# Kernel tuning notes

Measured on AMD Instinct MI355X. Metric: run time of the kernel, lower is better.

The kernel has to match this reference:

```python
import jax, jax.numpy as jnp
import numpy as np

NUM_EMBEDDINGS = 1024
EMBEDDING_DIM = 64
BETA = 0.25


def setup_inputs() -> dict:
    key = jax.random.key(0)
    k1, k2 = jax.random.split(key)
    z = jax.random.normal(k1, (64, 32, 32, EMBEDDING_DIM), dtype=jnp.float32)
    emb = jax.random.uniform(
        k2, (NUM_EMBEDDINGS, EMBEDDING_DIM), dtype=jnp.float32,
        minval=-1.0 / NUM_EMBEDDINGS, maxval=1.0 / NUM_EMBEDDINGS)
    return {"z": z, "emb": emb}


def reference(z, emb):
    zf = z.reshape(-1, EMBEDDING_DIM)                      # [N, D]
    # squared L2 distances via ||z||^2 - 2 z.e + ||e||^2  -> [N, K]
    distances = (jnp.sum(zf * zf, axis=1, keepdims=True)
                 - 2.0 * jnp.matmul(zf, emb.T)
                 + jnp.sum(emb * emb, axis=1))
    encoding_indices = jnp.argmin(distances, axis=1)       # [N]
    quantized = emb[encoding_indices].reshape(z.shape)     # [B, H, W, D]
    commitment_loss = BETA * jnp.mean((jax.lax.stop_gradient(quantized) - z) ** 2)
    codebook_loss = jnp.mean((quantized - jax.lax.stop_gradient(z)) ** 2)
    loss = commitment_loss + codebook_loss
    # straight-through estimator
    quantized = z + jax.lax.stop_gradient(quantized - z)
    return (quantized, loss)
```

## Files before the change

kernel.cpp:

```cpp
#include <hip/hip_runtime.h>
#include <stdint.h>

#define N_ROWS 65536
#define K_CODES 1024
#define D 64
#define OUT_ELEMS 4194304
#define LOSS_SCALE (1.25f / 4194304.0f)
#define ROWS_PER_BLOCK 128
#define GRID_DIST (N_ROWS / ROWS_PER_BLOCK)

typedef short short8 __attribute__((ext_vector_type(8)));
typedef float f32x4 __attribute__((ext_vector_type(4)));

__device__ __forceinline__ unsigned short f2bf(float f) {
    unsigned int u = __float_as_uint(f);
    return (unsigned short)((u + 0x7fffu + ((u >> 16) & 1u)) >> 16);
}

#define ECH (K_CODES * D / 8)
__global__ __launch_bounds__(256) void prep_kernel(const float* __restrict__ emb,
                                                   unsigned short* __restrict__ ebm2,
                                                   float* __restrict__ e2) {
    int t = blockIdx.x * 256 + threadIdx.x;
    if (t < ECH) {
        const float4* s = (const float4*)emb;
        float4 a = s[2 * t], b = s[2 * t + 1];
        uint4 o;
        o.x = f2bf(-2.f * a.x) | ((unsigned int)f2bf(-2.f * a.y) << 16);
        o.y = f2bf(-2.f * a.z) | ((unsigned int)f2bf(-2.f * a.w) << 16);
        o.z = f2bf(-2.f * b.x) | ((unsigned int)f2bf(-2.f * b.y) << 16);
        o.w = f2bf(-2.f * b.z) | ((unsigned int)f2bf(-2.f * b.w) << 16);
        ((uint4*)ebm2)[t] = o;
    } else if (t < ECH + K_CODES) {
        int k = t - ECH;
        const float4* e4 = (const float4*)emb;
        float s = 0.f;
#pragma unroll
        for (int i = 0; i < 16; i++) {
            float4 v = e4[k * 16 + i];
            s += v.x * v.x + v.y * v.y + v.z * v.z + v.w * v.w;
        }
        e2[k] = s;
    }
}

__global__ __launch_bounds__(256) void dist_fused_kernel(
        const float* __restrict__ z, const unsigned short* __restrict__ ebm2,
        const float* __restrict__ e2, const float* __restrict__ emb,
        float* __restrict__ out, float* __restrict__ partials) {
    const int tid = threadIdx.x;
    const int wave = tid >> 6, lane = tid & 63;
    const int n = lane & 15, q = lane >> 4;
    const int block_row0 = blockIdx.x * ROWS_PER_BLOCK;

    short8 b[2][2];
#pragma unroll
    for (int rs = 0; rs < 2; rs++) {
        const float* zr = z + (size_t)(block_row0 + wave * 32 + rs * 16 + n) * D + q * 8;
        float4 f0 = *(const float4*)(zr);
        float4 f1 = *(const float4*)(zr + 4);
        float4 f2 = *(const float4*)(zr + 32);
        float4 f3 = *(const float4*)(zr + 36);
        short8 lo, hi;
        lo[0] = f2bf(f0.x); lo[1] = f2bf(f0.y); lo[2] = f2bf(f0.z); lo[3] = f2bf(f0.w);
        lo[4] = f2bf(f1.x); lo[5] = f2bf(f1.y); lo[6] = f2bf(f1.z); lo[7] = f2bf(f1.w);
        hi[0] = f2bf(f2.x); hi[1] = f2bf(f2.y); hi[2] = f2bf(f2.z); hi[3] = f2bf(f2.w);
        hi[4] = f2bf(f3.x); hi[5] = f2bf(f3.y); hi[6] = f2bf(f3.z); hi[7] = f2bf(f3.w);
        b[rs][0] = lo; b[rs][1] = hi;
    }

    float bestd[2] = {INFINITY, INFINITY};
    int bestk[2] = {0, 0};

    short8 A0a, A1a, A0b, A1b;
    f32x4 Ea, Eb;
    {
        const unsigned short* er0 = ebm2 + (size_t)n * D + q * 8;
        A0a = *(const short8*)er0; A1a = *(const short8*)(er0 + 32);
        Ea = *(const f32x4*)(e2 + q * 4);
        const unsigned short* er1 = ebm2 + (size_t)(16 + n) * D + q * 8;
        A0b = *(const short8*)er1; A1b = *(const short8*)(er1 + 32);
        Eb = *(const f32x4*)(e2 + 16 + q * 4);
    }

    auto step = [&](int t, short8& A0, short8& A1, f32x4& E) {
        f32x4 acc0 = E, acc1 = E;
        acc0 = __builtin_amdgcn_mfma_f32_16x16x32_bf16(A0, b[0][0], acc0, 0, 0, 0);
        acc0 = __builtin_amdgcn_mfma_f32_16x16x32_bf16(A1, b[0][1], acc0, 0, 0, 0);
        acc1 = __builtin_amdgcn_mfma_f32_16x16x32_bf16(A0, b[1][0], acc1, 0, 0, 0);
        acc1 = __builtin_amdgcn_mfma_f32_16x16x32_bf16(A1, b[1][1], acc1, 0, 0, 0);
        int tp = (t + 2 > 63) ? 63 : (t + 2);
        const unsigned short* er = ebm2 + (size_t)(tp * 16 + n) * D + q * 8;
        A0 = *(const short8*)er;
        A1 = *(const short8*)(er + 32);
        E = *(const f32x4*)(e2 + tp * 16 + q * 4);
#pragma unroll
        for (int r = 0; r < 4; r++) {
            float d0 = acc0[r];
            if (d0 < bestd[0]) { bestd[0] = d0; bestk[0] = t * 16 + q * 4 + r; }
            float d1 = acc1[r];
            if (d1 < bestd[1]) { bestd[1] = d1; bestk[1] = t * 16 + q * 4 + r; }
        }
    };

    for (int t = 0; t < 64; t += 2) {
        step(t, A0a, A1a, Ea);
        step(t + 1, A0b, A1b, Eb);
    }

    __shared__ int sh_idx[ROWS_PER_BLOCK];
#pragma unroll
    for (int rs = 0; rs < 2; rs++) {
        unsigned int db = __float_as_uint(bestd[rs]);
        db = (db & 0x80000000u) ? ~db : (db | 0x80000000u);
        unsigned long long key = ((unsigned long long)db << 32) | (unsigned int)bestk[rs];
        unsigned long long o = __shfl_xor(key, 16, 64); key = o < key ? o : key;
        o = __shfl_xor(key, 32, 64); key = o < key ? o : key;
        if (q == 0) sh_idx[wave * 32 + rs * 16 + n] = (int)(key & 0xFFFFFFFFu);
    }
    __syncthreads();

    float ssum = 0.f;
    const float4* z4 = (const float4*)z;
    float4* o4 = (float4*)out;
#pragma unroll
    for (int it = 0; it < 8; it++) {
        int c = it * 256 + tid;
        int lrow = c >> 4, d4 = c & 15;
        int k = sh_idx[lrow];
        size_t gi = (size_t)block_row0 * 16 + c;
        float4 qv = ((const float4*)emb)[k * 16 + d4];
        float4 zv = z4[gi];
        o4[gi] = qv;
        float dx = qv.x - zv.x, dy = qv.y - zv.y, dz = qv.z - zv.z, dw = qv.w - zv.w;
        ssum += dx * dx + dy * dy + dz * dz + dw * dw;
    }
#pragma unroll
    for (int off = 32; off > 0; off >>= 1)
        ssum += __shfl_down(ssum, off, 64);
    __shared__ float ps[4];
    if (lane == 0) ps[wave] = ssum;
    __syncthreads();
    if (tid == 0) partials[blockIdx.x] = ps[0] + ps[1] + ps[2] + ps[3];
}

__global__ __launch_bounds__(256) void loss_kernel(const float* __restrict__ partials,
                                                   float* __restrict__ loss) {
    float s = partials[threadIdx.x] + partials[threadIdx.x + 256];
#pragma unroll
    for (int off = 32; off > 0; off >>= 1)
        s += __shfl_down(s, off, 64);
    __shared__ float ps[4];
    int wave = threadIdx.x >> 6, lane = threadIdx.x & 63;
    if (lane == 0) ps[wave] = s;
    __syncthreads();
    if (threadIdx.x == 0) loss[0] = (ps[0] + ps[1] + ps[2] + ps[3]) * LOSS_SCALE;
}

extern "C" void kernel_launch(void* const* d_in, const int* in_sizes, int n_in,
                              void* d_out, int out_size, void* d_ws, size_t ws_size,
                              hipStream_t stream) {
    const float* z = (const float*)d_in[0];
    const float* emb = (const float*)d_in[1];
    float* out = (float*)d_out;
    float* loss = out + OUT_ELEMS;

    char* ws = (char*)d_ws;
    float* e2 = (float*)ws;
    unsigned short* ebm2 = (unsigned short*)(ws + 4096);
    float* partials = (float*)(ws + 4096 + 131072 + 8192);

    prep_kernel<<<(ECH + K_CODES + 255) / 256, 256, 0, stream>>>(emb, ebm2, e2);
    dist_fused_kernel<<<GRID_DIST, 256, 0, stream>>>(z, ebm2, e2, emb, out, partials);
    loss_kernel<<<1, 256, 0, stream>>>(partials, loss);
}
```

Measured before the change: 109.8 us.

## Stage codebook into LDS via async global_load_lds with XOR swizzle double buffering

The kernel no longer has each wave read bf16 codebook fragments straight from global memory. It now copies the whole codebook into 64KB of shared memory in four 32KB chunks with global_load_lds, double-buffered, and uses an XOR swizzle to avoid bank conflicts on the MFMA operand reads. The goal is to cut redundant L2/global traffic, since all four waves previously fetched the same codebook rows. In exchange it adds block-wide barriers per chunk and a large LDS footprint, which caps occupancy at about two blocks per CU. It also reuses the staging buffer for the index and partial-sum scratch.

Measured after the change: 90.53 us. 1.21x faster.

```diff
diff --git a/kernel.cpp b/kernel.cpp
--- a/kernel.cpp
+++ b/kernel.cpp
@@ -16,6 +16,10 @@
     unsigned int u = __float_as_uint(f);
     return (unsigned short)((u + 0x7fffu + ((u >> 16) & 1u)) >> 16);
 }
+
+#define GLOAD_LDS16(g, l)                                                          \
+    __builtin_amdgcn_global_load_lds((const __attribute__((address_space(1))) void*)(g), \
+                                     (__attribute__((address_space(3))) void*)(l), 16, 0, 0)
 
 #define ECH (K_CODES * D / 8)
 __global__ __launch_bounds__(256) void prep_kernel(const float* __restrict__ emb,
@@ -44,13 +48,14 @@
     }
 }
 
-__global__ __launch_bounds__(256) void dist_fused_kernel(
+__global__ __launch_bounds__(256, 2) void dist_fused_kernel(
         const float* __restrict__ z, const unsigned short* __restrict__ ebm2,
         const float* __restrict__ e2, const float* __restrict__ emb,
         float* __restrict__ out, float* __restrict__ partials) {
+    __shared__ __align__(16) char smem[65536];
     const int tid = threadIdx.x;
     const int wave = tid >> 6, lane = tid & 63;
-    const int n = lane & 15, q = lane >> 4;
+    const int n = lane & 15, q = lane >> 4, nb = n & 7;
     const int block_row0 = blockIdx.x * ROWS_PER_BLOCK;
 
     short8 b[2][2];
@@ -69,46 +74,58 @@
         b[rs][0] = lo; b[rs][1] = hi;
     }
 
+    auto stage = [&](int c) {
+        const int bufoff = (c & 1) << 15;
+        const uint4* gsrc = (const uint4*)ebm2;
+#pragma unroll
+        for (int r = 0; r < 8; r++) {
+            int S = c * 2048 + r * 256 + tid;
+            int P = (S & ~7) | ((S & 7) ^ ((S >> 3) & 7));
+            char* l = smem + bufoff + (r * 256 + (tid & ~63)) * 16;
+            GLOAD_LDS16(gsrc + P, l);
+        }
+    };
+
+    f32x4 Ea = *(const f32x4*)(e2 + q * 4);
+    f32x4 Eb = *(const f32x4*)(e2 + 16 + q * 4);
+    const int base0 = n * 128 + ((q ^ nb) << 4);
+    const int base1 = n * 128 + (((4 | q) ^ nb) << 4);
+
     float bestd[2] = {INFINITY, INFINITY};
     int bestk[2] = {0, 0};
 
-    short8 A0a, A1a, A0b, A1b;
-    f32x4 Ea, Eb;
-    {
-        const unsigned short* er0 = ebm2 + (size_t)n * D + q * 8;
-        A0a = *(const short8*)er0; A1a = *(const short8*)(er0 + 32);
-        Ea = *(const f32x4*)(e2 + q * 4);
-        const unsigned short* er1 = ebm2 + (size_t)(16 + n) * D + q * 8;
-        A0b = *(const short8*)er1; A1b = *(const short8*)(er1 + 32);
-        Eb = *(const f32x4*)(e2 + 16 + q * 4);
+    stage(0);
+    __syncthreads();
+    for (int c = 0; c < 4; c++) {
+        if (c < 3) stage(c + 1);
+        const char* buf = smem + ((c & 1) << 15);
+#pragma unroll
+        for (int tl = 0; tl < 16; tl++) {
+            const int t = c * 16 + tl;
+            short8 a0 = *(const short8*)(buf + tl * 2048 + base0);
+            short8 a1 = *(const short8*)(buf + tl * 2048 + base1);
+            f32x4 E = (tl & 1) ? Eb : Ea;
+            f32x4 acc0 = E, acc1 = E;
+            acc0 = __builtin_amdgcn_mfma_f32_16x16x32_bf16(a0, b[0][0], acc0, 0, 0, 0);
+            acc0 = __builtin_amdgcn_mfma_f32_16x16x32_bf16(a1, b[0][1], acc0, 0, 0, 0);
+            acc1 = __builtin_amdgcn_mfma_f32_16x16x32_bf16(a0, b[1][0], acc1, 0, 0, 0);
+            acc1 = __builtin_amdgcn_mfma_f32_16x16x32_bf16(a1, b[1][1], acc1, 0, 0, 0);
+            int tp = (t + 2 > 63) ? 63 : (t + 2);
+            f32x4 En = *(const f32x4*)(e2 + tp * 16 + q * 4);
+            if (tl & 1) Eb = En; else Ea = En;
+#pragma unroll
+            for (int r = 0; r < 4; r++) {
+                float d0 = acc0[r];
+                if (d0 < bestd[0]) { bestd[0] = d0; bestk[0] = t * 16 + q * 4 + r; }
+                float d1 = acc1[r];
+                if (d1 < bestd[1]) { bestd[1] = d1; bestk[1] = t * 16 + q * 4 + r; }
+            }
+        }
+        __syncthreads();
     }
 
-    auto step = [&](int t, short8& A0, short8& A1, f32x4& E) {
-        f32x4 acc0 = E, acc1 = E;
-        acc0 = __builtin_amdgcn_mfma_f32_16x16x32_bf16(A0, b[0][0], acc0, 0, 0, 0);
-        acc0 = __builtin_amdgcn_mfma_f32_16x16x32_bf16(A1, b[0][1], acc0, 0, 0, 0);
-        acc1 = __builtin_amdgcn_mfma_f32_16x16x32_bf16(A0, b[1][0], acc1, 0, 0, 0);
-        acc1 = __builtin_amdgcn_mfma_f32_16x16x32_bf16(A1, b[1][1], acc1, 0, 0, 0);
-        int tp = (t + 2 > 63) ? 63 : (t + 2);
-        const unsigned short* er = ebm2 + (size_t)(tp * 16 + n) * D + q * 8;
-        A0 = *(const short8*)er;
-        A1 = *(const short8*)(er + 32);
-        E = *(const f32x4*)(e2 + tp * 16 + q * 4);
-#pragma unroll
-        for (int r = 0; r < 4; r++) {
-            float d0 = acc0[r];
-            if (d0 < bestd[0]) { bestd[0] = d0; bestk[0] = t * 16 + q * 4 + r; }
-            float d1 = acc1[r];
-            if (d1 < bestd[1]) { bestd[1] = d1; bestk[1] = t * 16 + q * 4 + r; }
-        }
-    };
-
-    for (int t = 0; t < 64; t += 2) {
-        step(t, A0a, A1a, Ea);
-        step(t + 1, A0b, A1b, Eb);
-    }
-
-    __shared__ int sh_idx[ROWS_PER_BLOCK];
+    int* sh_idx = (int*)smem;
+    float* ps = (float*)(smem + 512);
 #pragma unroll
     for (int rs = 0; rs < 2; rs++) {
         unsigned int db = __float_as_uint(bestd[rs]);
@@ -125,10 +142,10 @@
     float4* o4 = (float4*)out;
 #pragma unroll
     for (int it = 0; it < 8; it++) {
-        int c = it * 256 + tid;
-        int lrow = c >> 4, d4 = c & 15;
+        int cidx = it * 256 + tid;
+        int lrow = cidx >> 4, d4 = cidx & 15;
         int k = sh_idx[lrow];
-        size_t gi = (size_t)block_row0 * 16 + c;
+        size_t gi = (size_t)block_row0 * 16 + cidx;
         float4 qv = ((const float4*)emb)[k * 16 + d4];
         float4 zv = z4[gi];
         o4[gi] = qv;
@@ -138,7 +155,6 @@
 #pragma unroll
     for (int off = 32; off > 0; off >>= 1)
         ssum += __shfl_down(ssum, off, 64);
-    __shared__ float ps[4];
     if (lane == 0) ps[wave] = ssum;
     __syncthreads();
     if (tid == 0) partials[blockIdx.x] = ps[0] + ps[1] + ps[2] + ps[3];
```

## Hold codebook slice in registers per wave and stream z rows through it

Applied to the files above, without the earlier changes.

Removes the prep kernel. Each wave now converts its own quarter of the codebook to bf16 (scaled by -2) and computes the code norms, keeping the result in registers. The block then loops over 16-row chunks of z, and the four waves' partial argmins are combined through shared memory using packed distance|index keys. Quantized rows come from emb, and the loss is taken from the minimum distance instead of recomputing (q-z)^2. This saves a launch and the z re-read, but the distance keys lose mantissa precision (low 10 bits replaced by the index, plus a +1 offset), so argmin ties and the loss are approximated.

After: 113.9 us. 3.7% more time.

```diff
diff --git a/kernel.cpp b/kernel.cpp
--- a/kernel.cpp
+++ b/kernel.cpp
@@ -16,130 +16,122 @@
     unsigned int u = __float_as_uint(f);
     return (unsigned short)((u + 0x7fffu + ((u >> 16) & 1u)) >> 16);
 }
-
-#define ECH (K_CODES * D / 8)
-__global__ __launch_bounds__(256) void prep_kernel(const float* __restrict__ emb,
-                                                   unsigned short* __restrict__ ebm2,
-                                                   float* __restrict__ e2) {
-    int t = blockIdx.x * 256 + threadIdx.x;
-    if (t < ECH) {
-        const float4* s = (const float4*)emb;
-        float4 a = s[2 * t], b = s[2 * t + 1];
-        uint4 o;
-        o.x = f2bf(-2.f * a.x) | ((unsigned int)f2bf(-2.f * a.y) << 16);
-        o.y = f2bf(-2.f * a.z) | ((unsigned int)f2bf(-2.f * a.w) << 16);
-        o.z = f2bf(-2.f * b.x) | ((unsigned int)f2bf(-2.f * b.y) << 16);
-        o.w = f2bf(-2.f * b.z) | ((unsigned int)f2bf(-2.f * b.w) << 16);
-        ((uint4*)ebm2)[t] = o;
-    } else if (t < ECH + K_CODES) {
-        int k = t - ECH;
-        const float4* e4 = (const float4*)emb;
-        float s = 0.f;
-#pragma unroll
-        for (int i = 0; i < 16; i++) {
-            float4 v = e4[k * 16 + i];
-            s += v.x * v.x + v.y * v.y + v.z * v.z + v.w * v.w;
-        }
-        e2[k] = s;
-    }
+__device__ __forceinline__ short8 pack8(float4 a, float4 b) {
+    short8 r;
+    r[0] = f2bf(a.x); r[1] = f2bf(a.y); r[2] = f2bf(a.z); r[3] = f2bf(a.w);
+    r[4] = f2bf(b.x); r[5] = f2bf(b.y); r[6] = f2bf(b.z); r[7] = f2bf(b.w);
+    return r;
 }
 
-__global__ __launch_bounds__(256) void dist_fused_kernel(
-        const float* __restrict__ z, const unsigned short* __restrict__ ebm2,
-        const float* __restrict__ e2, const float* __restrict__ emb,
+__global__ __launch_bounds__(256, 2) void vq_kernel(
+        const float* __restrict__ z, const float* __restrict__ emb,
         float* __restrict__ out, float* __restrict__ partials) {
     const int tid = threadIdx.x;
-    const int wave = tid >> 6, lane = tid & 63;
+    const int w = tid >> 6, lane = tid & 63;
     const int n = lane & 15, q = lane >> 4;
-    const int block_row0 = blockIdx.x * ROWS_PER_BLOCK;
+    __shared__ unsigned int sh_key[2][4][16];
+    __shared__ float ps[4];
 
-    short8 b[2][2];
-#pragma unroll
-    for (int rs = 0; rs < 2; rs++) {
-        const float* zr = z + (size_t)(block_row0 + wave * 32 + rs * 16 + n) * D + q * 8;
-        float4 f0 = *(const float4*)(zr);
-        float4 f1 = *(const float4*)(zr + 4);
-        float4 f2 = *(const float4*)(zr + 32);
-        float4 f3 = *(const float4*)(zr + 36);
-        short8 lo, hi;
-        lo[0] = f2bf(f0.x); lo[1] = f2bf(f0.y); lo[2] = f2bf(f0.z); lo[3] = f2bf(f0.w);
-        lo[4] = f2bf(f1.x); lo[5] = f2bf(f1.y); lo[6] = f2bf(f1.z); lo[7] = f2bf(f1.w);
-        hi[0] = f2bf(f2.x); hi[1] = f2bf(f2.y); hi[2] = f2bf(f2.z); hi[3] = f2bf(f2.w);
-        hi[4] = f2bf(f3.x); hi[5] = f2bf(f3.y); hi[6] = f2bf(f3.z); hi[7] = f2bf(f3.w);
-        b[rs][0] = lo; b[rs][1] = hi;
+    const int r0 = blockIdx.x * ROWS_PER_BLOCK;
+
+    float4 c0, c1, c2, c3;
+    {
+        const float* zr = z + (size_t)(r0 + n) * D + q * 8;
+        c0 = *(const float4*)(zr);      c1 = *(const float4*)(zr + 4);
+        c2 = *(const float4*)(zr + 32); c3 = *(const float4*)(zr + 36);
     }
 
-    float bestd[2] = {INFINITY, INFINITY};
-    int bestk[2] = {0, 0};
-
-    short8 A0a, A1a, A0b, A1b;
-    f32x4 Ea, Eb;
-    {
-        const unsigned short* er0 = ebm2 + (size_t)n * D + q * 8;
-        A0a = *(const short8*)er0; A1a = *(const short8*)(er0 + 32);
-        Ea = *(const f32x4*)(e2 + q * 4);
-        const unsigned short* er1 = ebm2 + (size_t)(16 + n) * D + q * 8;
-        A0b = *(const short8*)er1; A1b = *(const short8*)(er1 + 32);
-        Eb = *(const f32x4*)(e2 + 16 + q * 4);
+    const int cbase = w * 256 + n;
+    short8 cb0[16], cb1[16];
+    float e2w[16];
+#pragma unroll
+    for (int ct = 0; ct < 16; ct++) {
+        const float* er = emb + (size_t)(cbase + ct * 16) * D + q * 8;
+        float4 g0 = *(const float4*)(er);      float4 g1 = *(const float4*)(er + 4);
+        float4 g2 = *(const float4*)(er + 32); float4 g3 = *(const float4*)(er + 36);
+        float e2p = g0.x*g0.x + g0.y*g0.y + g0.z*g0.z + g0.w*g0.w
+                  + g1.x*g1.x + g1.y*g1.y + g1.z*g1.z + g1.w*g1.w
+                  + g2.x*g2.x + g2.y*g2.y + g2.z*g2.z + g2.w*g2.w
+                  + g3.x*g3.x + g3.y*g3.y + g3.z*g3.z + g3.w*g3.w;
+        e2p += __shfl_xor(e2p, 16, 64);
+        e2p += __shfl_xor(e2p, 32, 64);
+        e2w[ct] = e2p + 1.0f;
+        float4 m0 = {-2.f*g0.x, -2.f*g0.y, -2.f*g0.z, -2.f*g0.w};
+        float4 m1 = {-2.f*g1.x, -2.f*g1.y, -2.f*g1.z, -2.f*g1.w};
+        float4 m2 = {-2.f*g2.x, -2.f*g2.y, -2.f*g2.z, -2.f*g2.w};
+        float4 m3 = {-2.f*g3.x, -2.f*g3.y, -2.f*g3.z, -2.f*g3.w};
+        cb0[ct] = pack8(m0, m1);
+        cb1[ct] = pack8(m2, m3);
     }
 
-    auto step = [&](int t, short8& A0, short8& A1, f32x4& E) {
-        f32x4 acc0 = E, acc1 = E;
-        acc0 = __builtin_amdgcn_mfma_f32_16x16x32_bf16(A0, b[0][0], acc0, 0, 0, 0);
-        acc0 = __builtin_amdgcn_mfma_f32_16x16x32_bf16(A1, b[0][1], acc0, 0, 0, 0);
-        acc1 = __builtin_amdgcn_mfma_f32_16x16x32_bf16(A0, b[1][0], acc1, 0, 0, 0);
-        acc1 = __builtin_amdgcn_mfma_f32_16x16x32_bf16(A1, b[1][1], acc1, 0, 0, 0);
-        int tp = (t + 2 > 63) ? 63 : (t + 2);
-        const unsigned short* er = ebm2 + (size_t)(tp * 16 + n) * D + q * 8;
-        A0 = *(const short8*)er;
-        A1 = *(const short8*)(er + 32);
-        E = *(const f32x4*)(e2 + tp * 16 + q * 4);
+    float lossacc = 0.f;
+    const float4* emb4 = (const float4*)emb;
+    float4* o4 = (float4*)out;
+
+    for (int s = 0; s < 8; s++) {
+        float z2p = c0.x*c0.x + c0.y*c0.y + c0.z*c0.z + c0.w*c0.w
+                  + c1.x*c1.x + c1.y*c1.y + c1.z*c1.z + c1.w*c1.w
+                  + c2.x*c2.x + c2.y*c2.y + c2.z*c2.z + c2.w*c2.w
+                  + c3.x*c3.x + c3.y*c3.y + c3.z*c3.z + c3.w*c3.w;
+        z2p += __shfl_xor(z2p, 16, 64);
+        z2p += __shfl_xor(z2p, 32, 64);
+        float z2r[4];
+#pragma unroll
+        for (int r = 0; r < 4; r++) z2r[r] = __shfl(z2p, q * 4 + r, 64);
+
+        short8 alo = pack8(c0, c1), ahi = pack8(c2, c3);
+
+        unsigned int best[4] = {~0u, ~0u, ~0u, ~0u};
+#pragma unroll
+        for (int ct = 0; ct < 16; ct++) {
+            f32x4 acc = {e2w[ct], e2w[ct], e2w[ct], e2w[ct]};
+            acc = __builtin_amdgcn_mfma_f32_16x16x32_bf16(alo, cb0[ct], acc, 0, 0, 0);
+            acc = __builtin_amdgcn_mfma_f32_16x16x32_bf16(ahi, cb1[ct], acc, 0, 0, 0);
+            const unsigned int id = (unsigned int)(cbase + ct * 16);
+#pragma unroll
+            for (int r = 0; r < 4; r++) {
+                unsigned int key = (__float_as_uint(acc[r] + z2r[r]) & 0xFFFFFC00u) | id;
+                best[r] = best[r] < key ? best[r] : key;
+            }
+        }
 #pragma unroll
         for (int r = 0; r < 4; r++) {
-            float d0 = acc0[r];
-            if (d0 < bestd[0]) { bestd[0] = d0; bestk[0] = t * 16 + q * 4 + r; }
-            float d1 = acc1[r];
-            if (d1 < bestd[1]) { bestd[1] = d1; bestk[1] = t * 16 + q * 4 + r; }
+#pragma unroll
+            for (int x = 1; x < 16; x <<= 1) {
+                unsigned int o = (unsigned int)__shfl_xor((int)best[r], x, 64);
+                best[r] = o < best[r] ? o : best[r];
+            }
         }
-    };
+        if (n == 0)
+            *(uint4*)&sh_key[s & 1][w][q << 2] =
+                make_uint4(best[0], best[1], best[2], best[3]);
 
-    for (int t = 0; t < 64; t += 2) {
-        step(t, A0a, A1a, Ea);
-        step(t + 1, A0b, A1b, Eb);
+        float4 n0, n1, n2, n3;
+        if (s < 7) {
+            const float* zr = z + (size_t)(r0 + (s + 1) * 16 + n) * D + q * 8;
+            n0 = *(const float4*)(zr);      n1 = *(const float4*)(zr + 4);
+            n2 = *(const float4*)(zr + 32); n3 = *(const float4*)(zr + 36);
+        }
+        __syncthreads();
+
+        {
+            const int row = tid >> 4, unit = tid & 15;
+            unsigned int k0 = sh_key[s & 1][0][row], k1 = sh_key[s & 1][1][row];
+            unsigned int k2 = sh_key[s & 1][2][row], k3 = sh_key[s & 1][3][row];
+            unsigned int ka = k0 < k1 ? k0 : k1, kb = k2 < k3 ? k2 : k3;
+            unsigned int km = ka < kb ? ka : kb;
+            int idx = (int)(km & 1023u);
+            o4[(size_t)(r0 + s * 16 + row) * 16 + unit] = emb4[idx * 16 + unit];
+            if (unit == 0)
+                lossacc += __uint_as_float(km & 0xFFFFFC00u) - 1.0f;
+        }
+        c0 = n0; c1 = n1; c2 = n2; c3 = n3;
     }
 
-    __shared__ int sh_idx[ROWS_PER_BLOCK];
-#pragma unroll
-    for (int rs = 0; rs < 2; rs++) {
-        unsigned int db = __float_as_uint(bestd[rs]);
-        db = (db & 0x80000000u) ? ~db : (db | 0x80000000u);
-        unsigned long long key = ((unsigned long long)db << 32) | (unsigned int)bestk[rs];
-        unsigned long long o = __shfl_xor(key, 16, 64); key = o < key ? o : key;
-        o = __shfl_xor(key, 32, 64); key = o < key ? o : key;
-        if (q == 0) sh_idx[wave * 32 + rs * 16 + n] = (int)(key & 0xFFFFFFFFu);
-    }
-    __syncthreads();
-
-    float ssum = 0.f;
-    const float4* z4 = (const float4*)z;
-    float4* o4 = (float4*)out;
-#pragma unroll
-    for (int it = 0; it < 8; it++) {
-        int c = it * 256 + tid;
-        int lrow = c >> 4, d4 = c & 15;
-        int k = sh_idx[lrow];
-        size_t gi = (size_t)block_row0 * 16 + c;
-        float4 qv = ((const float4*)emb)[k * 16 + d4];
-        float4 zv = z4[gi];
-        o4[gi] = qv;
-        float dx = qv.x - zv.x, dy = qv.y - zv.y, dz = qv.z - zv.z, dw = qv.w - zv.w;
-        ssum += dx * dx + dy * dy + dz * dz + dw * dw;
-    }
 #pragma unroll
     for (int off = 32; off > 0; off >>= 1)
-        ssum += __shfl_down(ssum, off, 64);
-    __shared__ float ps[4];
-    if (lane == 0) ps[wave] = ssum;
+        lossacc += __shfl_down(lossacc, off, 64);
+    if (lane == 0) ps[w] = lossacc;
     __syncthreads();
     if (tid == 0) partials[blockIdx.x] = ps[0] + ps[1] + ps[2] + ps[3];
 }
@@ -164,13 +156,8 @@
     const float* emb = (const float*)d_in[1];
     float* out = (float*)d_out;
     float* loss = out + OUT_ELEMS;
+    float* partials = (float*)d_ws;
 
-    char* ws = (char*)d_ws;
-    float* e2 = (float*)ws;
-    unsigned short* ebm2 = (unsigned short*)(ws + 4096);
-    float* partials = (float*)(ws + 4096 + 131072 + 8192);
-
-    prep_kernel<<<(ECH + K_CODES + 255) / 256, 256, 0, stream>>>(emb, ebm2, e2);
-    dist_fused_kernel<<<GRID_DIST, 256, 0, stream>>>(z, ebm2, e2, emb, out, partials);
+    vq_kernel<<<GRID_DIST, 256, 0, stream>>>(z, emb, out, partials);
     loss_kernel<<<1, 256, 0, stream>>>(partials, loss);
 }
```
